# Kernel tuning notes

Hardware: AMD Instinct MI355X
Metric: run time of the kernel (lower is better)

## Reference

```python
import jax, jax.numpy as jnp
import numpy as np

BN_EPS = 1e-5
BN_SCALE = 1.0 / np.sqrt(1.0 + BN_EPS).astype(np.float32)  # running_mean=0, running_var=1


def _conv1x1(x, w, b=None):
    y = jnp.einsum('bchw,oc->bohw', x, w)
    if b is not None:
        y = y + b.reshape(1, -1, 1, 1)
    return y


def _bn(x, g, b):
    # eval-mode BN with running_mean=0, running_var=1
    return x * (BN_SCALE * g).reshape(1, -1, 1, 1) + b.reshape(1, -1, 1, 1)


def _spatial_attn(x, w, b):
    avg = jnp.mean(x, axis=1, keepdims=True)
    mx = jnp.max(x, axis=1, keepdims=True)
    s = jnp.concatenate([avg, mx], axis=1)  # [B,2,H,W]
    y = jax.lax.conv_general_dilated(s, w, (1, 1), [(3, 3), (3, 3)],
                                     dimension_numbers=('NCHW', 'OIHW', 'NCHW'))
    return jax.nn.sigmoid(y + b.reshape(1, -1, 1, 1))  # [B,1,H,W]


def _channel_attn(x, w1, b1, w2, b2):
    avg = jnp.mean(x, axis=(2, 3))  # [B,C]
    mx = jnp.max(x, axis=(2, 3))
    fc = lambda v: jax.nn.relu(v @ w1.T + b1) @ w2.T + b2
    return jax.nn.sigmoid(fc(avg) + fc(mx))[:, :, None, None]  # [B,C,1,1]


def setup_inputs() -> dict:
    key = jax.random.key(0)
    B, C, H, W = 8, 256, 48, 48
    Cr, Cm = C // 8, C // 16
    ks = iter(jax.random.split(key, 24))
    n = lambda shape, scale=0.05: jax.random.normal(next(ks), shape, jnp.float32) * scale
    return dict(
        rgb=jax.random.normal(next(ks), (B, C, H, W), jnp.float32),
        chm=jax.random.normal(next(ks), (B, C, H, W), jnp.float32),
        rgb_sa_w=n((1, 2, 7, 7)), rgb_sa_b=jnp.zeros((1,), jnp.float32),
        chm_sa_w=n((1, 2, 7, 7)), chm_sa_b=jnp.zeros((1,), jnp.float32),
        rgb_fc1_w=n((Cm, C)), rgb_fc1_b=jnp.zeros((Cm,), jnp.float32),
        rgb_fc2_w=n((C, Cm)), rgb_fc2_b=jnp.zeros((C,), jnp.float32),
        chm_fc1_w=n((Cm, C)), chm_fc1_b=jnp.zeros((Cm,), jnp.float32),
        chm_fc2_w=n((C, Cm)), chm_fc2_b=jnp.zeros((C,), jnp.float32),
        rq_w=n((Cr, C)), rq_b=jnp.zeros((Cr,), jnp.float32),
        rk_w=n((Cr, C)), rk_b=jnp.zeros((Cr,), jnp.float32),
        rv_w=n((C, C)), rv_b=jnp.zeros((C,), jnp.float32),
        dq_w=n((Cr, C)), dq_b=jnp.zeros((Cr,), jnp.float32),
        dk_w=n((Cr, C)), dk_b=jnp.zeros((Cr,), jnp.float32),
        dv_w=n((C, C)), dv_b=jnp.zeros((C,), jnp.float32),
        gate_w=n((C, 2 * C)), gate_b=jnp.zeros((C,), jnp.float32),
        mlp1_w=n((24, C)), mlp1_g=jnp.ones((24,), jnp.float32), mlp1_b=jnp.zeros((24,), jnp.float32),
        mlp2_w=n((1, 24)), mlp2_g=jnp.ones((1,), jnp.float32), mlp2_b=jnp.zeros((1,), jnp.float32),
    )


def reference(rgb, chm, rgb_sa_w, rgb_sa_b, chm_sa_w, chm_sa_b,
              rgb_fc1_w, rgb_fc1_b, rgb_fc2_w, rgb_fc2_b,
              chm_fc1_w, chm_fc1_b, chm_fc2_w, chm_fc2_b,
              rq_w, rq_b, rk_w, rk_b, rv_w, rv_b,
              dq_w, dq_b, dk_w, dk_b, dv_w, dv_b,
              gate_w, gate_b, mlp1_w, mlp1_g, mlp1_b, mlp2_w, mlp2_g, mlp2_b):
    B, C, H, W = rgb.shape
    N = H * W
    Cr = rq_w.shape[0]
    scale = Cr ** -0.5

    # channel / spatial attentions
    rgb_sa = _spatial_attn(rgb, rgb_sa_w, rgb_sa_b)
    chm_sa = _spatial_attn(chm, chm_sa_w, chm_sa_b)
    rgb_ca = _channel_attn(rgb, rgb_fc1_w, rgb_fc1_b, rgb_fc2_w, rgb_fc2_b)
    chm_ca = _channel_attn(chm, chm_fc1_w, chm_fc1_b, chm_fc2_w, chm_fc2_b)

    attn_rgb = rgb * chm_sa * chm_ca
    attn_chm = chm * rgb_sa * rgb_ca

    # CAWF dual cross-modal attention
    flat = lambda x: x.reshape(B, -1, N)
    rq = flat(_conv1x1(rgb, rq_w, rq_b))   # [B,Cr,N]
    rk = flat(_conv1x1(rgb, rk_w, rk_b))
    rv = flat(_conv1x1(rgb, rv_w, rv_b))   # [B,C,N]
    dq = flat(_conv1x1(chm, dq_w, dq_b))
    dk = flat(_conv1x1(chm, dk_w, dk_b))
    dv = flat(_conv1x1(chm, dv_w, dv_b))

    rgb_attn = jax.nn.softmax(jnp.einsum('bcn,bcm->bnm', rq, dk) * scale, axis=-1)  # [B,N,N]
    chm_attn = jax.nn.softmax(jnp.einsum('bcn,bcm->bnm', dq, rk) * scale, axis=-1)
    rgb_att = jnp.einsum('bcn,bnm->bcm', rv, rgb_attn).reshape(B, C, H, W)
    chm_att = jnp.einsum('bcn,bnm->bcm', dv, chm_attn).reshape(B, C, H, W)

    c = jnp.concatenate([rgb_att, chm_att], axis=1)
    g = jax.nn.sigmoid(_conv1x1(c, gate_w, gate_b))
    c_fused = rgb_att * g + chm_att * (1.0 - g)
    d_fused = rgb_att * chm_att
    output = c_fused + d_fused

    h = jax.nn.relu(_bn(_conv1x1(output, mlp1_w), mlp1_g, mlp1_b))
    h = jax.nn.sigmoid(_bn(_conv1x1(h, mlp2_w), mlp2_g, mlp2_b))
    weight = jax.nn.sigmoid(h)  # double sigmoid as in original mlp (ConvBNSig + nn.Sigmoid)

    return attn_rgb + attn_chm * weight
```

## Files before the change

kernel.cpp:

```cpp
#include <hip/hip_runtime.h>
#include <hip/hip_bf16.h>
#include <cstdint>

#define DI __device__ __forceinline__

typedef float f32x4 __attribute__((ext_vector_type(4)));
typedef short bf16x8 __attribute__((ext_vector_type(8)));
typedef unsigned short u16x4 __attribute__((ext_vector_type(4)));

constexpr int B_ = 8, C_ = 256, HH = 48, WW = 48, N_ = 2304, CR = 32;
constexpr float QK_SCALE = 0.17677669529663687f;
constexpr float BN_SC = 0.99999500003749968f;

constexpr size_t QK_SZ   = (size_t)B_*N_*CR*2;
constexpr size_t V_SZ    = (size_t)B_*C_*N_*2;
constexpr size_t OFF_RQT = 0;
constexpr size_t OFF_RKT = OFF_RQT + QK_SZ;
constexpr size_t OFF_DQT = OFF_RKT + QK_SZ;
constexpr size_t OFF_DKT = OFF_DQT + QK_SZ;
constexpr size_t OFF_RV  = OFF_DKT + QK_SZ;
constexpr size_t OFF_DV  = OFF_RV + V_SZ;
constexpr size_t OFF_ATT = OFF_DV + V_SZ;
constexpr size_t ATT_SZ  = 2ull*B_*C_*N_*2;
constexpr size_t OFF_PCS = OFF_ATT;
constexpr size_t OFF_PCM = OFF_ATT + 2ull*8*36*256*4;
constexpr size_t OFF_SCONV = OFF_ATT + ATT_SZ;
constexpr size_t SCONV_SZ  = 2ull*B_*2*N_*4;
constexpr size_t OFF_SA    = OFF_SCONV + SCONV_SZ;
constexpr size_t SA_SZ     = 2ull*B_*N_*4;
constexpr size_t OFF_CA    = OFF_SA + SA_SZ;
constexpr size_t CST_SZ    = 2ull*B_*C_*4;
constexpr size_t OFF_WMAP  = OFF_CA + CST_SZ;
constexpr size_t OFF_WPROJ = OFF_WMAP + (size_t)B_*N_*4;
constexpr size_t WPROJ_SZ  = 2ull*320*256*2;
constexpr size_t OFF_WGATE = OFF_WPROJ + WPROJ_SZ;
constexpr size_t WS_NEEDED = OFF_WGATE + 256ull*512*2;

DI float bf2f(unsigned short u){ union{unsigned int i; float f;} v; v.i = ((unsigned int)u)<<16; return v.f; }
DI unsigned short f2bf(float f){ union{float f; unsigned int i;} v; v.f=f; unsigned int r = v.i + 0x7fffu + ((v.i>>16)&1u); return (unsigned short)(r>>16); }
DI float sigm(float x){ return 1.0f/(1.0f+__expf(-x)); }
DI u16x4 pk4(float p0, float p1, float p2, float p3){
  union { __hip_bfloat162 h[2]; u16x4 v; } u;
  u.h[0] = __float22bfloat162_rn(make_float2(p0, p1));
  u.h[1] = __float22bfloat162_rn(make_float2(p2, p3));
  return u.v;
}

__global__ void k_prep_w(const float* rq_w, const float* rk_w, const float* rv_w,
                         const float* dq_w, const float* dk_w, const float* dv_w,
                         const float* gate_w, unsigned short* wproj, unsigned short* wgate){
  int i = blockIdx.x*256 + threadIdx.x;
  if (i < 163840){
    int mod = i / 81920, r = (i >> 8) % 320, c = i & 255;
    const float* q = mod ? dq_w : rq_w;
    const float* k = mod ? dk_w : rk_w;
    const float* v = mod ? dv_w : rv_w;
    float val = (r < 32) ? q[r*256+c] : (r < 64 ? k[(r-32)*256+c] : v[(r-64)*256+c]);
    wproj[i] = f2bf(val);
  } else {
    int j = i - 163840;
    if (j < 131072) wgate[j] = f2bf(gate_w[j]);
  }
}

__global__ __launch_bounds__(256, 2) void k_stage(
                       const float* rgb, const float* chm, const unsigned short* wproj,
                       const float* rq_b, const float* rk_b, const float* rv_b,
                       const float* dq_b, const float* dk_b, const float* dv_b,
                       unsigned short* wsu, float* sconv, float* pcs, float* pcm){
  int mod = blockIdx.y;
  int b = blockIdx.x / 36, nt = blockIdx.x % 36;
  int pix0 = nt*64;
  const float* X = (mod ? chm : rgb) + (size_t)b*C_*N_ + pix0;
  __shared__ unsigned short xs[256*68];
  __shared__ float ls[4][64], lm[4][64];
  int t = threadIdx.x;
  {
    int srow = t >> 4;
    int scol = (t & 15) * 4;
    #pragma unroll
    for (int rr = 0; rr < 16; ++rr){
      int row = rr*16 + srow;
      float4 v = *(const float4*)(X + (size_t)row*N_ + scol);
      u16x4 h = { f2bf(v.x), f2bf(v.y), f2bf(v.z), f2bf(v.w) };
      *(u16x4*)(xs + row*68 + scol) = h;
    }
  }
  __syncthreads();
  {
    int p = t & 63, cg = t >> 6;
    float s = 0.f, mx = -INFINITY;
    for (int cc = 0; cc < 64; ++cc){
      float v = bf2f(xs[(cg*64+cc)*68 + p]);
      s += v; mx = fmaxf(mx, v);
    }
    ls[cg][p] = s; lm[cg][p] = mx;
  }
  {
    float cs = 0.f, cm = -INFINITY;
    for (int p = 0; p < 64; ++p){
      float v = bf2f(xs[t*68 + p]);
      cs += v; cm = fmaxf(cm, v);
    }
    pcs[((size_t)(mod*8+b)*36 + nt)*256 + t] = cs;
    pcm[((size_t)(mod*8+b)*36 + nt)*256 + t] = cm;
  }
  __syncthreads();
  if (t < 64){
    int p = t;
    float s = ls[0][p]+ls[1][p]+ls[2][p]+ls[3][p];
    float mx = fmaxf(fmaxf(lm[0][p],lm[1][p]), fmaxf(lm[2][p],lm[3][p]));
    sconv[((size_t)(mod*B_+b)*2 + 0)*N_ + pix0+p] = s*(1.f/256.f);
    sconv[((size_t)(mod*B_+b)*2 + 1)*N_ + pix0+p] = mx;
  }
  const unsigned short* Wm = wproj + (size_t)mod*320*256;
  int lane = t & 63, w = t >> 6;
  int l15 = lane & 15, g = lane >> 4;
  f32x4 acc[5][4];
  #pragma unroll
  for (int i = 0; i < 5; ++i)
    #pragma unroll
    for (int j = 0; j < 4; ++j) acc[i][j] = 0.f;
  for (int k0 = 0; k0 < 256; k0 += 32){
    bf16x8 af[5];
    #pragma unroll
    for (int cf = 0; cf < 5; ++cf)
      af[cf] = *(const bf16x8*)(Wm + (size_t)(w*80 + cf*16 + l15)*256 + k0 + g*8);
    bf16x8 bx[4];
    #pragma unroll
    for (int mf = 0; mf < 4; ++mf)
      #pragma unroll
      for (int j = 0; j < 8; ++j)
        bx[mf][j] = (short)xs[(k0 + g*8 + j)*68 + mf*16 + l15];
    #pragma unroll
    for (int cf = 0; cf < 5; ++cf)
      #pragma unroll
      for (int mf = 0; mf < 4; ++mf)
        acc[cf][mf] = __builtin_amdgcn_mfma_f32_16x16x32_bf16(af[cf], bx[mf], acc[cf][mf], 0, 0, 0);
  }
  const float* qb = mod ? dq_b : rq_b;
  const float* kb = mod ? dk_b : rk_b;
  const float* vb = mod ? dv_b : rv_b;
  unsigned short* qT = wsu + (mod ? OFF_DQT : OFF_RQT)/2;
  unsigned short* kT = wsu + (mod ? OFF_DKT : OFF_RKT)/2;
  unsigned short* vB = wsu + (mod ? OFF_DV  : OFF_RV )/2;
  #pragma unroll
  for (int cf = 0; cf < 5; ++cf){
    int base = w*80 + cf*16;
    #pragma unroll
    for (int mf = 0; mf < 4; ++mf){
      int col = pix0 + mf*16 + l15;
      if (base < 32){
        int o4 = base + g*4;
        u16x4 pk = { f2bf(acc[cf][mf][0] + qb[o4]),   f2bf(acc[cf][mf][1] + qb[o4+1]),
                     f2bf(acc[cf][mf][2] + qb[o4+2]), f2bf(acc[cf][mf][3] + qb[o4+3]) };
        *(u16x4*)(qT + (size_t)(b*N_ + col)*32 + o4) = pk;
      } else if (base < 64){
        int o4 = base - 32 + g*4;
        u16x4 pk = { f2bf(acc[cf][mf][0] + kb[o4]),   f2bf(acc[cf][mf][1] + kb[o4+1]),
                     f2bf(acc[cf][mf][2] + kb[o4+2]), f2bf(acc[cf][mf][3] + kb[o4+3]) };
        *(u16x4*)(kT + (size_t)(b*N_ + col)*32 + o4) = pk;
      } else {
        #pragma unroll
        for (int r = 0; r < 4; ++r){
          int o = base - 64 + g*4 + r;
          vB[((size_t)b*C_ + o)*N_ + col] = f2bf(acc[cf][mf][r] + vb[o]);
        }
      }
    }
  }
}

__global__ void k_sa_ca(const float* sconv, const float* rgb_sa_w, const float* rgb_sa_b,
                        const float* chm_sa_w, const float* chm_sa_b, float* sa,
                        const float* pcs, const float* pcm,
                        const float* rw1, const float* rb1, const float* rw2, const float* rb2,
                        const float* cw1, const float* cb1, const float* cw2, const float* cb2,
                        float* ca){
  int x = blockIdx.x;
  if (x < 144){
    int mod = x / 72;
    int idx = (x % 72)*256 + threadIdx.x;
    int b = idx / N_, pix = idx % N_;
    int y = pix / WW, xx0 = pix % WW;
    const float* w7 = mod ? chm_sa_w : rgb_sa_w;
    float acc = (mod ? chm_sa_b : rgb_sa_b)[0];
    const float* sin0 = sconv + (size_t)(mod*B_+b)*2*N_;
    #pragma unroll
    for (int ic = 0; ic < 2; ++ic)
      for (int ky = 0; ky < 7; ++ky){
        int yy = y + ky - 3; if (yy < 0 || yy >= HH) continue;
        for (int kx = 0; kx < 7; ++kx){
          int xx = xx0 + kx - 3; if (xx < 0 || xx >= WW) continue;
          acc += w7[(ic*7+ky)*7+kx] * sin0[ic*N_ + yy*WW + xx];
        }
      }
    sa[(mod*B_+b)*N_ + pix] = sigm(acc);
  } else {
    int y = x - 144;
    int mod = y >> 3, b = y & 7;
    const float* w1 = mod ? cw1 : rw1;  const float* b1 = mod ? cb1 : rb1;
    const float* w2 = mod ? cw2 : rw2;  const float* b2 = mod ? cb2 : rb2;
    __shared__ float va[256], vm[256], h1a[16], h1m[16];
    int t = threadIdx.x;
    float s = 0.f, mx = -INFINITY;
    for (int nt = 0; nt < 36; ++nt){
      s += pcs[((size_t)(mod*8+b)*36 + nt)*256 + t];
      mx = fmaxf(mx, pcm[((size_t)(mod*8+b)*36 + nt)*256 + t]);
    }
    va[t] = s*(1.f/(float)N_);
    vm[t] = mx;
    __syncthreads();
    if (t < 32){
      int j = t & 15;
      const float* v = (t >= 16) ? vm : va;
      float ss = b1[j];
      for (int c = 0; c < 256; ++c) ss += w1[j*256+c]*v[c];
      float* hp = (t >= 16) ? h1m : h1a;
      hp[j] = fmaxf(ss, 0.f);
    }
    __syncthreads();
    float fa = b2[t], fm = b2[t];
    #pragma unroll
    for (int j = 0; j < 16; ++j){ fa += w2[t*16+j]*h1a[j]; fm += w2[t*16+j]*h1m[j]; }
    ca[(mod*B_+b)*C_ + t] = sigm(fa + fm);
  }
}

__global__ void k_phase_a(unsigned short* wsu){
  int orig = blockIdx.x;
  int b = orig & 7;
  int logical = orig >> 3;
  int a = logical / 36;
  int nb0 = (logical % 36)*64;
  int lane = threadIdx.x & 63, w = threadIdx.x >> 6;
  int l15 = lane & 15, g = lane >> 4;
  int n0 = nb0 + w*16;
  const unsigned short* Q = wsu + (a ? OFF_DQT : OFF_RQT)/2;
  const unsigned short* K = wsu + (a ? OFF_RKT : OFF_DKT)/2;
  bf16x8 af = *(const bf16x8*)(Q + (size_t)(b*N_ + n0 + l15)*32 + g*8);
  float lrun[4] = {0.f,0.f,0.f,0.f};
  for (int m0 = 0; m0 < N_; m0 += 64){
    f32x4 d[4];
    #pragma unroll
    for (int s = 0; s < 4; ++s){
      bf16x8 bk = *(const bf16x8*)(K + (size_t)(b*N_ + m0 + s*16 + l15)*32 + g*8);
      f32x4 z = 0.f;
      d[s] = __builtin_amdgcn_mfma_f32_16x16x32_bf16(af, bk, z, 0, 0, 0);
    }
    #pragma unroll
    for (int r = 0; r < 4; ++r)
      lrun[r] += (__expf(d[0][r]*QK_SCALE)+__expf(d[1][r]*QK_SCALE))
               + (__expf(d[2][r]*QK_SCALE)+__expf(d[3][r]*QK_SCALE));
  }
  #pragma unroll
  for (int r = 0; r < 4; ++r)
    #pragma unroll
    for (int msk = 1; msk < 16; msk <<= 1) lrun[r] += __shfl_xor(lrun[r], msk);
  __shared__ float lsv[64];
  if (l15 == 0){
    #pragma unroll
    for (int r = 0; r < 4; ++r) lsv[w*16 + g*4 + r] = 1.0f / lrun[r];
  }
  __syncthreads();
  unsigned short* V = wsu + (a ? OFF_DV : OFF_RV)/2 + ((size_t)b*C_ + threadIdx.x)*N_ + nb0;
  #pragma unroll
  for (int j8 = 0; j8 < 8; ++j8){
    bf16x8 vv = *(const bf16x8*)(V + j8*8);
    bf16x8 ov;
    #pragma unroll
    for (int e = 0; e < 8; ++e)
      ov[e] = (short)f2bf(bf2f((unsigned short)vv[e]) * lsv[j8*8 + e]);
    *(bf16x8*)(V + j8*8) = ov;
  }
}

__global__ __launch_bounds__(256, 3) void k_pv5(
                          const unsigned short* wsu, unsigned short* att){
  int orig = blockIdx.x;
  int logical = (orig & 7)*72 + (orig >> 3);
  int pair = logical / 36, mblk = logical % 36;
  int a = pair >> 3, b = pair & 7;
  int m0 = mblk*64;
  int lane = threadIdx.x & 63, w = threadIdx.x >> 6;
  int l15 = lane & 15, g = lane >> 4;
  int qm  = (w & 1)*32;
  int qnn = (w >> 1)*64;
  const unsigned short* Q = wsu + (a ? OFF_DQT : OFF_RQT)/2;
  const unsigned short* K = wsu + (a ? OFF_RKT : OFF_DKT)/2;
  const unsigned short* V = wsu + (a ? OFF_DV  : OFF_RV )/2;
  __shared__ __align__(16) unsigned char plds[2][64*256];

  bf16x8 kb[2];
  #pragma unroll
  for (int s = 0; s < 2; ++s)
    kb[s] = *(const bf16x8*)(K + (size_t)(b*N_ + m0 + qm + s*16 + l15)*32 + g*8);

  f32x4 acc[4][4];
  #pragma unroll
  for (int i = 0; i < 4; ++i)
    #pragma unroll
    for (int j = 0; j < 4; ++j) acc[i][j] = 0.f;

  auto computePh = [&](int n0base, int buf, int half){
    #pragma unroll
    for (int fi = 0; fi < 2; ++fi){
      int fr = half*2 + fi;
      int nb = n0base + qnn + fr*16;
      bf16x8 qa = *(const bf16x8*)(Q + (size_t)(b*N_ + nb + l15)*32 + g*8);
      #pragma unroll
      for (int fm = 0; fm < 2; ++fm){
        f32x4 z = 0.f;
        f32x4 d = __builtin_amdgcn_mfma_f32_16x16x32_bf16(qa, kb[fm], z, 0, 0, 0);
        int ml = qm + fm*16 + l15;
        int nl = qnn + fr*16 + g*4;
        u16x4 pk = pk4(__expf(d[0]*QK_SCALE), __expf(d[1]*QK_SCALE),
                       __expf(d[2]*QK_SCALE), __expf(d[3]*QK_SCALE));
        *(u16x4*)(plds[buf] + ml*256 + ((nl*2) ^ ((ml&7)<<4))) = pk;
      }
    }
  };

  computePh(0, 0, 0);
  computePh(0, 0, 1);
  __syncthreads();
  for (int t = 0; t < 18; ++t){
    int n0 = t*128;
    const unsigned char* pbuf = plds[t & 1];
    #pragma unroll
    for (int s = 0; s < 4; ++s){
      bf16x8 pb[4];
      #pragma unroll
      for (int mf = 0; mf < 4; ++mf){
        int ml = mf*16 + l15;
        pb[mf] = *(const bf16x8*)(pbuf + ml*256 + ((s*64 + g*16) ^ ((ml&7)<<4)));
      }
      bf16x8 av[4];
      #pragma unroll
      for (int cf = 0; cf < 4; ++cf)
        av[cf] = *(const bf16x8*)(V + ((size_t)b*C_ + w*64 + cf*16 + l15)*N_ + n0 + s*32 + g*8);
      if (t < 17 && s < 2) computePh(n0 + 128, (t+1)&1, s);
      __builtin_amdgcn_s_setprio(1);
      #pragma unroll
      for (int cf = 0; cf < 4; ++cf)
        #pragma unroll
        for (int mf = 0; mf < 4; ++mf)
          acc[cf][mf] = __builtin_amdgcn_mfma_f32_16x16x32_bf16(av[cf], pb[mf], acc[cf][mf], 0, 0, 0);
      __builtin_amdgcn_s_setprio(0);
    }
    __syncthreads();
  }
  unsigned short* ap = att + (((size_t)a*8 + b)*256)*N_;
  #pragma unroll
  for (int cf = 0; cf < 4; ++cf)
    #pragma unroll
    for (int mf = 0; mf < 4; ++mf)
      #pragma unroll
      for (int r = 0; r < 4; ++r){
        int c = w*64 + cf*16 + g*4 + r;
        int m = m0 + mf*16 + l15;
        ap[(size_t)c*N_ + m] = f2bf(acc[cf][mf][r]);
      }
}

__global__ __launch_bounds__(256, 2) void k_gatemlp(
                           const unsigned short* att, const unsigned short* wgate,
                           const float* gate_b,
                           const float* w1, const float* g1, const float* b1,
                           const float* w2, const float* g2, const float* b2,
                           float* wmap){
  int b = blockIdx.y, m0 = blockIdx.x*32;
  int lane = threadIdx.x & 63, w = threadIdx.x >> 6;
  int l15 = lane & 15, g = lane >> 4;
  __shared__ unsigned short ats[32][520];
  __shared__ unsigned short fvs[256][34];
  __shared__ float hs[24][33];
  int row8 = threadIdx.x >> 3;
  int mq = (threadIdx.x & 7)*4;
  for (int rb = 0; rb < 16; ++rb){
    int k = rb*32 + row8;
    int aa = k >> 8, c = k & 255;
    size_t base = (((size_t)aa*8 + b)*256 + c)*N_ + m0 + mq;
    u16x4 p0 = *(const u16x4*)(att + base);
    #pragma unroll
    for (int j = 0; j < 4; ++j) ats[mq + j][k] = p0[j];
  }
  __syncthreads();
  f32x4 acc[4][2];
  #pragma unroll
  for (int i = 0; i < 4; ++i){ acc[i][0] = 0.f; acc[i][1] = 0.f; }
  for (int k0 = 0; k0 < 512; k0 += 32){
    bf16x8 aw[4], bt[2];
    #pragma unroll
    for (int of = 0; of < 4; ++of)
      aw[of] = *(const bf16x8*)(wgate + (size_t)(w*64 + of*16 + l15)*512 + k0 + g*8);
    #pragma unroll
    for (int mf = 0; mf < 2; ++mf)
      bt[mf] = *(const bf16x8*)(&ats[mf*16 + l15][k0 + g*8]);
    #pragma unroll
    for (int of = 0; of < 4; ++of)
      #pragma unroll
      for (int mf = 0; mf < 2; ++mf)
        acc[of][mf] = __builtin_amdgcn_mfma_f32_16x16x32_bf16(aw[of], bt[mf], acc[of][mf], 0, 0, 0);
  }
  #pragma unroll
  for (int of = 0; of < 4; ++of){
    int o4 = w*64 + of*16 + g*4;
    float4 gb4 = *(const float4*)(gate_b + o4);
    #pragma unroll
    for (int mf = 0; mf < 2; ++mf){
      int ml = mf*16 + l15;
      u16x4 ra4 = *(const u16x4*)(&ats[ml][o4]);
      u16x4 da4 = *(const u16x4*)(&ats[ml][256 + o4]);
      #pragma unroll
      for (int r = 0; r < 4; ++r){
        float gg = sigm(acc[of][mf][r] + (&gb4.x)[r]);
        float ra = bf2f(ra4[r]);
        float da = bf2f(da4[r]);
        float fv = ra*gg + da*(1.f - gg) + ra*da;
        fvs[o4 + r][ml] = f2bf(fv);
      }
    }
  }
  __syncthreads();
  {
    int m = threadIdx.x & 31, jg = threadIdx.x >> 5;
    const float* w1r0 = w1 + (size_t)(jg*3+0)*256;
    const float* w1r1 = w1 + (size_t)(jg*3+1)*256;
    const float* w1r2 = w1 + (size_t)(jg*3+2)*256;
    float h0 = 0.f, h1 = 0.f, h2 = 0.f;
    for (int c = 0; c < 256; ++c){
      float v = bf2f(fvs[c][m]);
      h0 += w1r0[c]*v; h1 += w1r1[c]*v; h2 += w1r2[c]*v;
    }
    hs[jg*3+0][m] = h0; hs[jg*3+1][m] = h1; hs[jg*3+2][m] = h2;
  }
  __syncthreads();
  if (threadIdx.x < 32){
    int mm = threadIdx.x;
    float s2 = 0.f;
    #pragma unroll
    for (int j = 0; j < 24; ++j){
      float hj = fmaxf(hs[j][mm]*(BN_SC*g1[j]) + b1[j], 0.f);
      s2 += w2[j]*hj;
    }
    s2 = s2*(BN_SC*g2[0]) + b2[0];
    wmap[b*N_ + m0 + mm] = sigm(sigm(s2));
  }
}

__global__ void k_final(const float* rgb, const float* chm, const float* sa, const float* ca,
                        const float* wmap, float* out){
  const int total4 = B_*C_*N_/4;
  for (int i = blockIdx.x*blockDim.x + threadIdx.x; i < total4; i += gridDim.x*blockDim.x){
    int e = i*4;
    int b = e / (C_*N_);
    int rem = e % (C_*N_);
    int c = rem / N_;
    int pix = rem % N_;
    float4 rv = *(const float4*)(rgb + e);
    float4 cv = *(const float4*)(chm + e);
    float4 sc = *(const float4*)(sa + (size_t)(B_ + b)*N_ + pix);
    float4 sr = *(const float4*)(sa + (size_t)b*N_ + pix);
    float4 wm = *(const float4*)(wmap + (size_t)b*N_ + pix);
    float cac = ca[(B_ + b)*C_ + c];
    float car = ca[b*C_ + c];
    float4 o;
    o.x = rv.x*sc.x*cac + cv.x*sr.x*car*wm.x;
    o.y = rv.y*sc.y*cac + cv.y*sr.y*car*wm.y;
    o.z = rv.z*sc.z*cac + cv.z*sr.z*car*wm.z;
    o.w = rv.w*sc.w*cac + cv.w*sr.w*car*wm.w;
    *(float4*)(out + e) = o;
  }
}

extern "C" void kernel_launch(void* const* d_in, const int* in_sizes, int n_in,
                              void* d_out, int out_size, void* d_ws, size_t ws_size,
                              hipStream_t stream){
  if (ws_size < WS_NEEDED) return;
  const float* rgb      = (const float*)d_in[0];
  const float* chm      = (const float*)d_in[1];
  const float* rgb_sa_w = (const float*)d_in[2];
  const float* rgb_sa_b = (const float*)d_in[3];
  const float* chm_sa_w = (const float*)d_in[4];
  const float* chm_sa_b = (const float*)d_in[5];
  const float* rgb_fc1_w= (const float*)d_in[6];
  const float* rgb_fc1_b= (const float*)d_in[7];
  const float* rgb_fc2_w= (const float*)d_in[8];
  const float* rgb_fc2_b= (const float*)d_in[9];
  const float* chm_fc1_w= (const float*)d_in[10];
  const float* chm_fc1_b= (const float*)d_in[11];
  const float* chm_fc2_w= (const float*)d_in[12];
  const float* chm_fc2_b= (const float*)d_in[13];
  const float* rq_w = (const float*)d_in[14];
  const float* rq_b = (const float*)d_in[15];
  const float* rk_w = (const float*)d_in[16];
  const float* rk_b = (const float*)d_in[17];
  const float* rv_w = (const float*)d_in[18];
  const float* rv_b = (const float*)d_in[19];
  const float* dq_w = (const float*)d_in[20];
  const float* dq_b = (const float*)d_in[21];
  const float* dk_w = (const float*)d_in[22];
  const float* dk_b = (const float*)d_in[23];
  const float* dv_w = (const float*)d_in[24];
  const float* dv_b = (const float*)d_in[25];
  const float* gate_w = (const float*)d_in[26];
  const float* gate_b = (const float*)d_in[27];
  const float* mlp1_w = (const float*)d_in[28];
  const float* mlp1_g = (const float*)d_in[29];
  const float* mlp1_b = (const float*)d_in[30];
  const float* mlp2_w = (const float*)d_in[31];
  const float* mlp2_g = (const float*)d_in[32];
  const float* mlp2_b = (const float*)d_in[33];

  char* ws = (char*)d_ws;
  unsigned short* wsu   = (unsigned short*)d_ws;
  float* sconv = (float*)(ws + OFF_SCONV);
  float* sa    = (float*)(ws + OFF_SA);
  float* ca    = (float*)(ws + OFF_CA);
  float* wmap  = (float*)(ws + OFF_WMAP);
  float* pcs   = (float*)(ws + OFF_PCS);
  float* pcm   = (float*)(ws + OFF_PCM);
  unsigned short* wproj = (unsigned short*)(ws + OFF_WPROJ);
  unsigned short* wgate = (unsigned short*)(ws + OFF_WGATE);
  unsigned short* att   = (unsigned short*)(ws + OFF_ATT);

  k_prep_w<<<dim3(1152), dim3(256), 0, stream>>>(rq_w, rk_w, rv_w, dq_w, dk_w, dv_w, gate_w, wproj, wgate);
  k_stage<<<dim3(288,2), dim3(256), 0, stream>>>(rgb, chm, wproj, rq_b, rk_b, rv_b, dq_b, dk_b, dv_b,
                                                 wsu, sconv, pcs, pcm);
  k_sa_ca<<<dim3(160), dim3(256), 0, stream>>>(sconv, rgb_sa_w, rgb_sa_b, chm_sa_w, chm_sa_b, sa,
                                               pcs, pcm, rgb_fc1_w, rgb_fc1_b, rgb_fc2_w, rgb_fc2_b,
                                               chm_fc1_w, chm_fc1_b, chm_fc2_w, chm_fc2_b, ca);
  k_phase_a<<<dim3(576), dim3(256), 0, stream>>>(wsu);
  k_pv5<<<dim3(576), dim3(256), 0, stream>>>(wsu, att);
  k_gatemlp<<<dim3(72,8), dim3(256), 0, stream>>>(att, wgate, gate_b,
                                                  mlp1_w, mlp1_g, mlp1_b, mlp2_w, mlp2_g, mlp2_b, wmap);
  k_final<<<dim3(2048), dim3(256), 0, stream>>>(rgb, chm, sa, ca, wmap, (float*)d_out);
}
```

Measured before the change: 260.0 us.

## Fuse final blend into gate-MLP kernel and prefetch V in PV loop

Removes the separate k_final launch and the wmap buffer: each k_gatemlp block now computes its 32-pixel weight map into shared memory and directly writes the output for all 256 channels of those pixels. This drops one launch and the wmap round trip. In the PV kernel, V fragments are now double-buffered in registers and loaded one step ahead, and the LDS XOR swizzle widens from 8 to 16 rows to cut bank conflicts. The fused epilogue adds serial work to a kernel with only 576 blocks, and the V prefetch raises register pressure.

```diff
diff --git a/kernel.cpp b/kernel.cpp
--- a/kernel.cpp
+++ b/kernel.cpp
@@ -30,8 +30,7 @@
 constexpr size_t SA_SZ     = 2ull*B_*N_*4;
 constexpr size_t OFF_CA    = OFF_SA + SA_SZ;
 constexpr size_t CST_SZ    = 2ull*B_*C_*4;
-constexpr size_t OFF_WMAP  = OFF_CA + CST_SZ;
-constexpr size_t OFF_WPROJ = OFF_WMAP + (size_t)B_*N_*4;
+constexpr size_t OFF_WPROJ = OFF_CA + CST_SZ;
 constexpr size_t WPROJ_SZ  = 2ull*320*256*2;
 constexpr size_t OFF_WGATE = OFF_WPROJ + WPROJ_SZ;
 constexpr size_t WS_NEEDED = OFF_WGATE + 256ull*512*2;
@@ -316,10 +315,12 @@
         int nl = qnn + fr*16 + g*4;
         u16x4 pk = pk4(__expf(d[0]*QK_SCALE), __expf(d[1]*QK_SCALE),
                        __expf(d[2]*QK_SCALE), __expf(d[3]*QK_SCALE));
-        *(u16x4*)(plds[buf] + ml*256 + ((nl*2) ^ ((ml&7)<<4))) = pk;
+        *(u16x4*)(plds[buf] + ml*256 + ((nl*2) ^ ((ml&15)<<4))) = pk;
       }
     }
   };
+
+  const unsigned short* Vb = V + ((size_t)b*C_ + w*64 + l15)*N_;
 
   computePh(0, 0, 0);
   computePh(0, 0, 1);
@@ -327,26 +328,33 @@
   for (int t = 0; t < 18; ++t){
     int n0 = t*128;
     const unsigned char* pbuf = plds[t & 1];
+    bf16x8 av[2][4];
+    #pragma unroll
+    for (int ss = 0; ss < 2; ++ss)
+      #pragma unroll
+      for (int cf = 0; cf < 4; ++cf)
+        av[ss][cf] = *(const bf16x8*)(Vb + (size_t)cf*16*N_ + n0 + ss*32 + g*8);
     #pragma unroll
     for (int s = 0; s < 4; ++s){
       bf16x8 pb[4];
       #pragma unroll
       for (int mf = 0; mf < 4; ++mf){
         int ml = mf*16 + l15;
-        pb[mf] = *(const bf16x8*)(pbuf + ml*256 + ((s*64 + g*16) ^ ((ml&7)<<4)));
-      }
-      bf16x8 av[4];
-      #pragma unroll
-      for (int cf = 0; cf < 4; ++cf)
-        av[cf] = *(const bf16x8*)(V + ((size_t)b*C_ + w*64 + cf*16 + l15)*N_ + n0 + s*32 + g*8);
+        pb[mf] = *(const bf16x8*)(pbuf + ml*256 + ((s*64 + g*16) ^ ((ml&15)<<4)));
+      }
       if (t < 17 && s < 2) computePh(n0 + 128, (t+1)&1, s);
       __builtin_amdgcn_s_setprio(1);
       #pragma unroll
       for (int cf = 0; cf < 4; ++cf)
         #pragma unroll
         for (int mf = 0; mf < 4; ++mf)
-          acc[cf][mf] = __builtin_amdgcn_mfma_f32_16x16x32_bf16(av[cf], pb[mf], acc[cf][mf], 0, 0, 0);
+          acc[cf][mf] = __builtin_amdgcn_mfma_f32_16x16x32_bf16(av[s&1][cf], pb[mf], acc[cf][mf], 0, 0, 0);
       __builtin_amdgcn_s_setprio(0);
+      if (s < 2){
+        #pragma unroll
+        for (int cf = 0; cf < 4; ++cf)
+          av[s][cf] = *(const bf16x8*)(Vb + (size_t)cf*16*N_ + n0 + (s+2)*32 + g*8);
+      }
     }
     __syncthreads();
   }
@@ -368,13 +376,15 @@
                            const float* gate_b,
                            const float* w1, const float* g1, const float* b1,
                            const float* w2, const float* g2, const float* b2,
-                           float* wmap){
+                           const float* rgb, const float* chm, const float* sa, const float* ca,
+                           float* out){
   int b = blockIdx.y, m0 = blockIdx.x*32;
   int lane = threadIdx.x & 63, w = threadIdx.x >> 6;
   int l15 = lane & 15, g = lane >> 4;
   __shared__ unsigned short ats[32][520];
   __shared__ unsigned short fvs[256][34];
   __shared__ float hs[24][33];
+  __shared__ float swm[32], ssr[32], ssc[32];
   int row8 = threadIdx.x >> 3;
   int mq = (threadIdx.x & 7)*4;
   for (int rb = 0; rb < 16; ++rb){
@@ -445,32 +455,28 @@
       s2 += w2[j]*hj;
     }
     s2 = s2*(BN_SC*g2[0]) + b2[0];
-    wmap[b*N_ + m0 + mm] = sigm(sigm(s2));
-  }
-}
-
-__global__ void k_final(const float* rgb, const float* chm, const float* sa, const float* ca,
-                        const float* wmap, float* out){
-  const int total4 = B_*C_*N_/4;
-  for (int i = blockIdx.x*blockDim.x + threadIdx.x; i < total4; i += gridDim.x*blockDim.x){
-    int e = i*4;
-    int b = e / (C_*N_);
-    int rem = e % (C_*N_);
-    int c = rem / N_;
-    int pix = rem % N_;
-    float4 rv = *(const float4*)(rgb + e);
-    float4 cv = *(const float4*)(chm + e);
-    float4 sc = *(const float4*)(sa + (size_t)(B_ + b)*N_ + pix);
-    float4 sr = *(const float4*)(sa + (size_t)b*N_ + pix);
-    float4 wm = *(const float4*)(wmap + (size_t)b*N_ + pix);
-    float cac = ca[(B_ + b)*C_ + c];
-    float car = ca[b*C_ + c];
-    float4 o;
-    o.x = rv.x*sc.x*cac + cv.x*sr.x*car*wm.x;
-    o.y = rv.y*sc.y*cac + cv.y*sr.y*car*wm.y;
-    o.z = rv.z*sc.z*cac + cv.z*sr.z*car*wm.z;
-    o.w = rv.w*sc.w*cac + cv.w*sr.w*car*wm.w;
-    *(float4*)(out + e) = o;
+    swm[mm] = sigm(sigm(s2));
+    ssr[mm] = sa[(size_t)b*N_ + m0 + mm];
+    ssc[mm] = sa[(size_t)(B_+b)*N_ + m0 + mm];
+  }
+  __syncthreads();
+  {
+    int c8 = threadIdx.x >> 3;
+    int p4 = (threadIdx.x & 7)*4;
+    for (int pass = 0; pass < 8; ++pass){
+      int c = pass*32 + c8;
+      float cac = ca[(B_+b)*C_ + c];
+      float car = ca[b*C_ + c];
+      size_t off = ((size_t)b*C_ + c)*N_ + m0 + p4;
+      float4 rv4 = *(const float4*)(rgb + off);
+      float4 cv4 = *(const float4*)(chm + off);
+      float4 o;
+      o.x = rv4.x*ssc[p4+0]*cac + cv4.x*ssr[p4+0]*car*swm[p4+0];
+      o.y = rv4.y*ssc[p4+1]*cac + cv4.y*ssr[p4+1]*car*swm[p4+1];
+      o.z = rv4.z*ssc[p4+2]*cac + cv4.z*ssr[p4+2]*car*swm[p4+2];
+      o.w = rv4.w*ssc[p4+3]*cac + cv4.w*ssr[p4+3]*car*swm[p4+3];
+      *(float4*)(out + off) = o;
+    }
   }
 }
 
@@ -518,7 +524,6 @@
   float* sconv = (float*)(ws + OFF_SCONV);
   float* sa    = (float*)(ws + OFF_SA);
   float* ca    = (float*)(ws + OFF_CA);
-  float* wmap  = (float*)(ws + OFF_WMAP);
   float* pcs   = (float*)(ws + OFF_PCS);
   float* pcm   = (float*)(ws + OFF_PCM);
   unsigned short* wproj = (unsigned short*)(ws + OFF_WPROJ);
@@ -534,6 +539,6 @@
   k_phase_a<<<dim3(576), dim3(256), 0, stream>>>(wsu);
   k_pv5<<<dim3(576), dim3(256), 0, stream>>>(wsu, att);
   k_gatemlp<<<dim3(72,8), dim3(256), 0, stream>>>(att, wgate, gate_b,
-                                                  mlp1_w, mlp1_g, mlp1_b, mlp2_w, mlp2_g, mlp2_b, wmap);
-  k_final<<<dim3(2048), dim3(256), 0, stream>>>(rgb, chm, sa, ca, wmap, (float*)d_out);
-}
+                                                  mlp1_w, mlp1_g, mlp1_b, mlp2_w, mlp2_g, mlp2_b,
+                                                  rgb, chm, sa, ca, (float*)d_out);
+}
```

Measured after the change: 266.1 us. +2.4%, slower.
